# Performance work log

Measured on AMD Instinct MI355X. Metric: run time of the kernel, lower is better.

Reference implementation:

```python
import jax, jax.numpy as jnp
import numpy as np

EMB = 1024
E = 8        # num_experts
TOPK = 2
HID = 2048   # expert_dim

def setup_inputs() -> dict:
    key = jax.random.key(0)
    ks = jax.random.split(key, 10)
    s = lambda fan_in: 1.0 / np.sqrt(fan_in)
    x  = jax.random.normal(ks[0], (2, 2048, EMB), dtype=jnp.float32)
    Wr = jax.random.normal(ks[1], (EMB, E), dtype=jnp.float32) * s(EMB)
    br = jnp.zeros((E,), dtype=jnp.float32)
    # stacked expert weights, stored (in, out) so y = x @ W + b
    W1 = jax.random.normal(ks[2], (E, EMB, HID), dtype=jnp.float32) * s(EMB)
    b1 = jax.random.normal(ks[3], (E, HID), dtype=jnp.float32) * 0.01
    Wg = jax.random.normal(ks[4], (E, HID, HID), dtype=jnp.float32) * s(HID)
    bg = jax.random.normal(ks[5], (E, HID), dtype=jnp.float32) * 0.01
    W2 = jax.random.normal(ks[6], (E, HID, EMB), dtype=jnp.float32) * s(HID)
    b2 = jax.random.normal(ks[7], (E, EMB), dtype=jnp.float32) * 0.01
    return {"x": x, "Wr": Wr, "br": br, "W1": W1, "b1": b1,
            "Wg": Wg, "bg": bg, "W2": W2, "b2": b2}

def reference(x, Wr, br, W1, b1, Wg, bg, W2, b2):
    B, S, D = x.shape
    xt = x.reshape(B * S, D)                                  # [T, D]
    logits = xt @ Wr + br                                     # [T, E]
    probs = jax.nn.softmax(logits, axis=-1)
    topk_p, topk_i = jax.lax.top_k(probs, TOPK)               # [T, K]
    # dense gate matrix (top-k probs, NOT renormalized, as in source)
    gates = jnp.sum(jax.nn.one_hot(topk_i, E, dtype=xt.dtype) * topk_p[..., None], axis=1)  # [T, E]
    # expert MLP: layer1 (no act) -> relu(linear) -> layer2, for all experts
    h = jnp.einsum('td,edh->teh', xt, W1) + b1                # [T, E, HID]
    h = jax.nn.relu(jnp.einsum('teh,ehg->teg', h, Wg) + bg)   # [T, E, HID]
    y = jnp.einsum('teh,ehd->ted', h, W2) + b2                # [T, E, D]
    out = jnp.einsum('te,ted->td', gates, y)                  # weighted combine
    return out.reshape(B, S, D)
```

## Files before the change

### kernel.cpp

```cpp
#include <hip/hip_runtime.h>
#include <hip/hip_bf16.h>
#include <stdint.h>

#define NTOK 4096
#define EMBD 1024
#define NEXP 8
#define HIDD 2048
#define NPAIR (NTOK * 2)

typedef __attribute__((ext_vector_type(8))) __bf16 bf16x8;
typedef __attribute__((ext_vector_type(4))) float f32x4;

union V16 { uint4 u; bf16x8 b; };

__device__ __forceinline__ uint16_t f2bf(float f) {
    uint32_t u = __float_as_uint(f);
    return (uint16_t)((u + 0x7FFFu + ((u >> 16) & 1u)) >> 16);
}
__device__ __forceinline__ float bf2f(uint16_t u) {
    return __uint_as_float(((uint32_t)u) << 16);
}
__device__ __forceinline__ void gl_lds16(const uint16_t* g, uint16_t* l) {
    __builtin_amdgcn_global_load_lds(
        (const __attribute__((address_space(1))) void*)g,
        (__attribute__((address_space(3))) void*)l, 16, 0, 0);
}

#define W1_TILES 4096
#define WG_TILES 8192
#define W2_TILES 4096
__global__ __launch_bounds__(256) void transcast3_kernel(
    const float* __restrict__ W1, const float* __restrict__ Wg,
    const float* __restrict__ W2, uint16_t* __restrict__ W1t,
    uint16_t* __restrict__ Wgt, uint16_t* __restrict__ W2t) {
    int id = blockIdx.x;
    const float* src; uint16_t* dst; int K, N;
    if (id < W1_TILES) { src = W1; dst = W1t; K = EMBD; N = HIDD; }
    else if (id < W1_TILES + WG_TILES) { id -= W1_TILES; src = Wg; dst = Wgt; K = HIDD; N = HIDD; }
    else { id -= W1_TILES + WG_TILES; src = W2; dst = W2t; K = HIDD; N = EMBD; }
    int tn = N >> 6, tk = K >> 6;
    int per_e = tn * tk;
    int e = id / per_e, r = id % per_e;
    int n0 = (r % tn) * 64, k0 = (r / tn) * 64;

    __shared__ uint16_t tile[64][68];
    const float* S = src + ((size_t)e * K + k0) * N + n0;
    uint16_t* D = dst + ((size_t)e * N + n0) * K + k0;
    int t = threadIdx.x;
    int rn = (t & 15) * 4, rk = t >> 4;
#pragma unroll
    for (int p = 0; p < 4; p++) {
        int k = rk + p * 16;
        float4 v = *(const float4*)(S + (size_t)k * N + rn);
        ushort4 o;
        o.x = f2bf(v.x); o.y = f2bf(v.y); o.z = f2bf(v.z); o.w = f2bf(v.w);
        *(ushort4*)&tile[k][rn] = o;
    }
    __syncthreads();
    int wn = t >> 3, wk = (t & 7) * 8;
#pragma unroll
    for (int p = 0; p < 2; p++) {
        int n = wn + p * 32;
        uint32_t w0 = (uint32_t)tile[wk + 0][n] | ((uint32_t)tile[wk + 1][n] << 16);
        uint32_t w1 = (uint32_t)tile[wk + 2][n] | ((uint32_t)tile[wk + 3][n] << 16);
        uint32_t w2 = (uint32_t)tile[wk + 4][n] | ((uint32_t)tile[wk + 5][n] << 16);
        uint32_t w3 = (uint32_t)tile[wk + 6][n] | ((uint32_t)tile[wk + 7][n] << 16);
        uint4 pk = {w0, w1, w2, w3};
        *(uint4*)(D + (size_t)n * K + wk) = pk;
    }
}

__global__ __launch_bounds__(64) void router_kernel(const float* __restrict__ x,
                                                    const float* __restrict__ Wr,
                                                    const float* __restrict__ br,
                                                    uint16_t* __restrict__ xb,
                                                    int* __restrict__ counts,
                                                    int* __restrict__ pair_e,
                                                    float* __restrict__ pair_p) {
    int tok = blockIdx.x;
    int lane = threadIdx.x;
    const float* xr = x + (size_t)tok * EMBD;
    uint16_t* xbr = xb + (size_t)tok * EMBD;
    float acc[NEXP];
#pragma unroll
    for (int e = 0; e < NEXP; e++) acc[e] = 0.f;
    for (int d = lane; d < EMBD; d += 64) {
        float xv = xr[d];
        xbr[d] = f2bf(xv);
#pragma unroll
        for (int e = 0; e < NEXP; e++) acc[e] += xv * Wr[d * NEXP + e];
    }
#pragma unroll
    for (int e = 0; e < NEXP; e++) {
#pragma unroll
        for (int off = 32; off > 0; off >>= 1)
            acc[e] += __shfl_down(acc[e], off, 64);
    }
    if (lane == 0) {
        float lg[NEXP];
#pragma unroll
        for (int e = 0; e < NEXP; e++) lg[e] = acc[e] + br[e];
        int e0 = 0;
#pragma unroll
        for (int e = 1; e < NEXP; e++) if (lg[e] > lg[e0]) e0 = e;
        int e1 = (e0 == 0) ? 1 : 0;
#pragma unroll
        for (int e = 0; e < NEXP; e++) if (e != e0 && lg[e] > lg[e1]) e1 = e;
        float mx = lg[0];
#pragma unroll
        for (int e = 1; e < NEXP; e++) mx = fmaxf(mx, lg[e]);
        float s = 0.f, p[NEXP];
#pragma unroll
        for (int e = 0; e < NEXP; e++) { p[e] = __expf(lg[e] - mx); s += p[e]; }
        float inv = 1.f / s;
        pair_e[tok * 2 + 0] = e0; pair_p[tok * 2 + 0] = p[e0] * inv;
        pair_e[tok * 2 + 1] = e1; pair_p[tok * 2 + 1] = p[e1] * inv;
        atomicAdd(&counts[e0], 1);
        atomicAdd(&counts[e1], 1);
    }
}

__global__ __launch_bounds__(256) void scatter_kernel(const int* __restrict__ pair_e,
                                                      const int* __restrict__ counts,
                                                      int* __restrict__ cursors,
                                                      int* __restrict__ toklist,
                                                      int* __restrict__ posmap) {
    int i = blockIdx.x * 256 + threadIdx.x;
    int e = pair_e[i];
    int offs = 0;
    for (int j = 0; j < NEXP; j++) offs += (j < e) ? counts[j] : 0;
    int pos = offs + atomicAdd(&cursors[e], 1);
    toklist[pos] = i >> 1;
    posmap[i] = pos;
}

template <int KDIM, int NDIM, bool GATHER_A, bool RELU>
__global__ __launch_bounds__(256) void gemm_kernel(
    const uint16_t* __restrict__ Abase, const uint16_t* __restrict__ Btbase,
    const float* __restrict__ bbase, uint16_t* __restrict__ Out,
    const int* __restrict__ counts, const int* __restrict__ toklist) {
    int e = blockIdx.z;
    int offs = 0;
    for (int j = 0; j < NEXP; j++) offs += (j < e) ? counts[j] : 0;
    int n_e = counts[e];
    int m0 = blockIdx.y * 128;
    if (m0 >= n_e) return;
    int n0 = blockIdx.x * 128;
    const uint16_t* Bt = Btbase + (size_t)e * NDIM * KDIM;

    __shared__ uint16_t As[128 * 32];
    __shared__ uint16_t Bs[128 * 32];

    int tid = threadIdx.x;
    int lane = tid & 63;
    int wave = tid >> 6;

    int sr = tid >> 2;
    int ss = tid & 3;
    const uint16_t* arp[2];
    const uint16_t* brp[2];
#pragma unroll
    for (int p = 0; p < 2; p++) {
        int r = p * 64 + sr;
        int gs = ss ^ ((r >> 1) & 3);
        int grow;
        if (GATHER_A) {
            int idx = m0 + r;
            if (idx >= n_e) idx = 0;
            grow = toklist[offs + idx];
        } else {
            grow = offs + m0 + r;
        }
        arp[p] = Abase + (size_t)grow * KDIM + gs * 8;
        brp[p] = Bt + (size_t)(n0 + r) * KDIM + gs * 8;
    }
    uint16_t* alds[2] = { &As[wave * 512], &As[2048 + wave * 512] };
    uint16_t* blds[2] = { &Bs[wave * 512], &Bs[2048 + wave * 512] };

    int wm = (wave >> 1) * 64;
    int wn = (wave & 1) * 64;
    int l16 = lane & 15, qd = lane >> 4;
    const uint16_t* afp[4];
    const uint16_t* bfp[4];
#pragma unroll
    for (int t = 0; t < 4; t++) {
        int ar = wm + t * 16 + l16;
        afp[t] = &As[ar * 32 + (qd ^ ((ar >> 1) & 3)) * 8];
        int br = wn + t * 16 + l16;
        bfp[t] = &Bs[br * 32 + (qd ^ ((br >> 1) & 3)) * 8];
    }

    f32x4 acc[4][4];
    f32x4 zero = {0.f, 0.f, 0.f, 0.f};
#pragma unroll
    for (int i = 0; i < 4; i++)
#pragma unroll
        for (int j = 0; j < 4; j++) acc[i][j] = zero;

    for (int kb = 0; kb < KDIM; kb += 32) {
#pragma unroll
        for (int p = 0; p < 2; p++) {
            gl_lds16(arp[p] + kb, alds[p]);
            gl_lds16(brp[p] + kb, blds[p]);
        }
        __syncthreads();
        V16 af[4], bf[4];
#pragma unroll
        for (int t = 0; t < 4; t++) {
            af[t].u = *(const uint4*)(afp[t]);
            bf[t].u = *(const uint4*)(bfp[t]);
        }
#pragma unroll
        for (int i = 0; i < 4; i++)
#pragma unroll
            for (int j = 0; j < 4; j++)
                acc[i][j] = __builtin_amdgcn_mfma_f32_16x16x32_bf16(
                    af[i].b, bf[j].b, acc[i][j], 0, 0, 0);
        __syncthreads();
    }

    const float* bias = bbase + (size_t)e * NDIM;
    int mrem = n_e - m0;
#pragma unroll
    for (int i = 0; i < 4; i++) {
        int rb = wm + i * 16 + qd * 4;
#pragma unroll
        for (int j = 0; j < 4; j++) {
            int col = n0 + wn + j * 16 + l16;
            float bv = bias[col];
#pragma unroll
            for (int r = 0; r < 4; r++) {
                int lr = rb + r;
                if (lr < mrem) {
                    float v = acc[i][j][r] + bv;
                    if (RELU) v = fmaxf(v, 0.f);
                    Out[(size_t)(offs + m0 + lr) * NDIM + col] = f2bf(v);
                }
            }
        }
    }
}

__global__ __launch_bounds__(256) void combine_kernel(const uint16_t* __restrict__ y,
                                                      const int* __restrict__ posmap,
                                                      const float* __restrict__ pair_p,
                                                      float* __restrict__ out) {
    int t = blockIdx.x;
    int d4 = threadIdx.x;
    int p0 = posmap[t * 2], p1 = posmap[t * 2 + 1];
    float w0 = pair_p[t * 2], w1 = pair_p[t * 2 + 1];
    ushort4 a = ((const ushort4*)(y + (size_t)p0 * EMBD))[d4];
    ushort4 b = ((const ushort4*)(y + (size_t)p1 * EMBD))[d4];
    float4 o;
    o.x = w0 * bf2f(a.x) + w1 * bf2f(b.x);
    o.y = w0 * bf2f(a.y) + w1 * bf2f(b.y);
    o.z = w0 * bf2f(a.z) + w1 * bf2f(b.z);
    o.w = w0 * bf2f(a.w) + w1 * bf2f(b.w);
    ((float4*)(out + (size_t)t * EMBD))[d4] = o;
}

extern "C" void kernel_launch(void* const* d_in, const int* in_sizes, int n_in,
                              void* d_out, int out_size, void* d_ws, size_t ws_size,
                              hipStream_t stream) {
    const float* x  = (const float*)d_in[0];
    const float* Wr = (const float*)d_in[1];
    const float* br = (const float*)d_in[2];
    const float* W1 = (const float*)d_in[3];
    const float* b1 = (const float*)d_in[4];
    const float* Wg = (const float*)d_in[5];
    const float* bg = (const float*)d_in[6];
    const float* W2 = (const float*)d_in[7];
    const float* b2 = (const float*)d_in[8];
    float* out = (float*)d_out;

    char* ws = (char*)d_ws;
    uint16_t* xb  = (uint16_t*)ws;
    uint16_t* h   = (uint16_t*)(ws + (8ull << 20));
    uint16_t* yb  = h;
    uint16_t* W1t = (uint16_t*)(ws + (40ull << 20));
    uint16_t* g   = W1t;
    uint16_t* Wgt = (uint16_t*)(ws + (72ull << 20));
    uint16_t* W2t = (uint16_t*)(ws + (136ull << 20));
    int* meta = (int*)(ws + (168ull << 20));
    int*   counts  = meta;
    int*   cursors = meta + 8;
    int*   pair_e  = meta + 16;
    int*   toklist = meta + 16 + NPAIR;
    int*   posmap  = meta + 16 + 2 * NPAIR;
    float* pair_p  = (float*)(meta + 16 + 3 * NPAIR);

    hipMemsetAsync(counts, 0, 16 * sizeof(int), stream);

    router_kernel<<<NTOK, 64, 0, stream>>>(x, Wr, br, xb, counts, pair_e, pair_p);
    transcast3_kernel<<<W1_TILES + WG_TILES + W2_TILES, 256, 0, stream>>>(
        W1, Wg, W2, W1t, Wgt, W2t);
    scatter_kernel<<<NPAIR / 256, 256, 0, stream>>>(pair_e, counts, cursors, toklist, posmap);

    gemm_kernel<EMBD, HIDD, true, false>
        <<<dim3(HIDD / 128, NTOK / 128, NEXP), 256, 0, stream>>>(
            xb, W1t, b1, h, counts, toklist);
    gemm_kernel<HIDD, HIDD, false, true>
        <<<dim3(HIDD / 128, NTOK / 128, NEXP), 256, 0, stream>>>(
            h, Wgt, bg, g, counts, toklist);
    gemm_kernel<HIDD, EMBD, false, false>
        <<<dim3(EMBD / 128, NTOK / 128, NEXP), 256, 0, stream>>>(
            g, W2t, b2, yb, counts, toklist);
    combine_kernel<<<NTOK, 256, 0, stream>>>(yb, posmap, pair_p, out);
}
```

Measured before the change: 737.1 us.

## Fuse fp32 weight cast and transpose into GEMM B-tile loading

Removes the separate pre-pass that cast and transposed every expert weight matrix to bf16 in workspace. Each GEMM block now reads the original fp32 weights, converts them to bf16 in registers and writes them transposed into a padded LDS tile, prefetching the next k-slice into registers. This avoids one full read and write pass over all weights, about 384 MB of traffic. In exchange each M-block re-reads fp32 weights, doubling per-block B bandwidth, and relies on L2/MALL reuse. The LDS writes are unswizzled, so bank conflicts are possible.

Result: slower. 804.9 us (+9.2%).

```diff
diff --git a/kernel.cpp b/kernel.cpp
--- a/kernel.cpp
+++ b/kernel.cpp
@@ -17,6 +17,9 @@
     uint32_t u = __float_as_uint(f);
     return (uint16_t)((u + 0x7FFFu + ((u >> 16) & 1u)) >> 16);
 }
+__device__ __forceinline__ uint32_t pk2bf(float a, float b) {
+    return (uint32_t)f2bf(a) | ((uint32_t)f2bf(b) << 16);
+}
 __device__ __forceinline__ float bf2f(uint16_t u) {
     return __uint_as_float(((uint32_t)u) << 16);
 }
@@ -24,50 +27,6 @@
     __builtin_amdgcn_global_load_lds(
         (const __attribute__((address_space(1))) void*)g,
         (__attribute__((address_space(3))) void*)l, 16, 0, 0);
-}
-
-#define W1_TILES 4096
-#define WG_TILES 8192
-#define W2_TILES 4096
-__global__ __launch_bounds__(256) void transcast3_kernel(
-    const float* __restrict__ W1, const float* __restrict__ Wg,
-    const float* __restrict__ W2, uint16_t* __restrict__ W1t,
-    uint16_t* __restrict__ Wgt, uint16_t* __restrict__ W2t) {
-    int id = blockIdx.x;
-    const float* src; uint16_t* dst; int K, N;
-    if (id < W1_TILES) { src = W1; dst = W1t; K = EMBD; N = HIDD; }
-    else if (id < W1_TILES + WG_TILES) { id -= W1_TILES; src = Wg; dst = Wgt; K = HIDD; N = HIDD; }
-    else { id -= W1_TILES + WG_TILES; src = W2; dst = W2t; K = HIDD; N = EMBD; }
-    int tn = N >> 6, tk = K >> 6;
-    int per_e = tn * tk;
-    int e = id / per_e, r = id % per_e;
-    int n0 = (r % tn) * 64, k0 = (r / tn) * 64;
-
-    __shared__ uint16_t tile[64][68];
-    const float* S = src + ((size_t)e * K + k0) * N + n0;
-    uint16_t* D = dst + ((size_t)e * N + n0) * K + k0;
-    int t = threadIdx.x;
-    int rn = (t & 15) * 4, rk = t >> 4;
-#pragma unroll
-    for (int p = 0; p < 4; p++) {
-        int k = rk + p * 16;
-        float4 v = *(const float4*)(S + (size_t)k * N + rn);
-        ushort4 o;
-        o.x = f2bf(v.x); o.y = f2bf(v.y); o.z = f2bf(v.z); o.w = f2bf(v.w);
-        *(ushort4*)&tile[k][rn] = o;
-    }
-    __syncthreads();
-    int wn = t >> 3, wk = (t & 7) * 8;
-#pragma unroll
-    for (int p = 0; p < 2; p++) {
-        int n = wn + p * 32;
-        uint32_t w0 = (uint32_t)tile[wk + 0][n] | ((uint32_t)tile[wk + 1][n] << 16);
-        uint32_t w1 = (uint32_t)tile[wk + 2][n] | ((uint32_t)tile[wk + 3][n] << 16);
-        uint32_t w2 = (uint32_t)tile[wk + 4][n] | ((uint32_t)tile[wk + 5][n] << 16);
-        uint32_t w3 = (uint32_t)tile[wk + 6][n] | ((uint32_t)tile[wk + 7][n] << 16);
-        uint4 pk = {w0, w1, w2, w3};
-        *(uint4*)(D + (size_t)n * K + wk) = pk;
-    }
 }
 
 __global__ __launch_bounds__(64) void router_kernel(const float* __restrict__ x,
@@ -136,7 +95,7 @@
 
 template <int KDIM, int NDIM, bool GATHER_A, bool RELU>
 __global__ __launch_bounds__(256) void gemm_kernel(
-    const uint16_t* __restrict__ Abase, const uint16_t* __restrict__ Btbase,
+    const uint16_t* __restrict__ Abase, const float* __restrict__ Wbase,
     const float* __restrict__ bbase, uint16_t* __restrict__ Out,
     const int* __restrict__ counts, const int* __restrict__ toklist) {
     int e = blockIdx.z;
@@ -146,10 +105,10 @@
     int m0 = blockIdx.y * 128;
     if (m0 >= n_e) return;
     int n0 = blockIdx.x * 128;
-    const uint16_t* Bt = Btbase + (size_t)e * NDIM * KDIM;
+    const float* W = Wbase + (size_t)e * KDIM * NDIM;
 
     __shared__ uint16_t As[128 * 32];
-    __shared__ uint16_t Bs[128 * 32];
+    __shared__ uint16_t Bs[128 * 36];
 
     int tid = threadIdx.x;
     int lane = tid & 63;
@@ -158,7 +117,6 @@
     int sr = tid >> 2;
     int ss = tid & 3;
     const uint16_t* arp[2];
-    const uint16_t* brp[2];
 #pragma unroll
     for (int p = 0; p < 2; p++) {
         int r = p * 64 + sr;
@@ -172,10 +130,13 @@
             grow = offs + m0 + r;
         }
         arp[p] = Abase + (size_t)grow * KDIM + gs * 8;
-        brp[p] = Bt + (size_t)(n0 + r) * KDIM + gs * 8;
     }
     uint16_t* alds[2] = { &As[wave * 512], &As[2048 + wave * 512] };
-    uint16_t* blds[2] = { &Bs[wave * 512], &Bs[2048 + wave * 512] };
+
+    int nq = tid & 31;
+    int kq = tid >> 5;
+    const float* Wp = W + (size_t)(kq * 4) * NDIM + n0 + nq * 4;
+    uint16_t* bwp = &Bs[(nq * 4) * 36 + kq * 4];
 
     int wm = (wave >> 1) * 64;
     int wn = (wave & 1) * 64;
@@ -187,7 +148,7 @@
         int ar = wm + t * 16 + l16;
         afp[t] = &As[ar * 32 + (qd ^ ((ar >> 1) & 3)) * 8];
         int br = wn + t * 16 + l16;
-        bfp[t] = &Bs[br * 32 + (qd ^ ((br >> 1) & 3)) * 8];
+        bfp[t] = &Bs[br * 36 + qd * 8];
     }
 
     f32x4 acc[4][4];
@@ -197,18 +158,39 @@
 #pragma unroll
         for (int j = 0; j < 4; j++) acc[i][j] = zero;
 
+    float4 breg[4];
+#pragma unroll
+    for (int j = 0; j < 4; j++)
+        breg[j] = *(const float4*)(Wp + (size_t)j * NDIM);
+
     for (int kb = 0; kb < KDIM; kb += 32) {
 #pragma unroll
-        for (int p = 0; p < 2; p++) {
-            gl_lds16(arp[p] + kb, alds[p]);
-            gl_lds16(brp[p] + kb, blds[p]);
-        }
+        for (int p = 0; p < 2; p++) gl_lds16(arp[p] + kb, alds[p]);
+#pragma unroll
+        for (int i = 0; i < 4; i++) {
+            uint2 d;
+            d.x = pk2bf(breg[0].x, breg[1].x);
+            d.y = pk2bf(breg[2].x, breg[3].x);
+            *(uint2*)(bwp + i * 36) = d;
+            float4 t0 = breg[0], t1 = breg[1], t2 = breg[2], t3 = breg[3];
+            breg[0] = make_float4(t0.y, t0.z, t0.w, t0.x);
+            breg[1] = make_float4(t1.y, t1.z, t1.w, t1.x);
+            breg[2] = make_float4(t2.y, t2.z, t2.w, t2.x);
+            breg[3] = make_float4(t3.y, t3.z, t3.w, t3.x);
+        }
+        int kbn = (kb + 32 < KDIM) ? kb + 32 : 0;
+        float4 bnext[4];
+#pragma unroll
+        for (int j = 0; j < 4; j++)
+            bnext[j] = *(const float4*)(Wp + (size_t)(kbn + j) * NDIM);
         __syncthreads();
         V16 af[4], bf[4];
 #pragma unroll
         for (int t = 0; t < 4; t++) {
             af[t].u = *(const uint4*)(afp[t]);
-            bf[t].u = *(const uint4*)(bfp[t]);
+            uint2 lo = *(const uint2*)(bfp[t]);
+            uint2 hi = *(const uint2*)(bfp[t] + 4);
+            bf[t].u = make_uint4(lo.x, lo.y, hi.x, hi.y);
         }
 #pragma unroll
         for (int i = 0; i < 4; i++)
@@ -217,6 +199,8 @@
                 acc[i][j] = __builtin_amdgcn_mfma_f32_16x16x32_bf16(
                     af[i].b, bf[j].b, acc[i][j], 0, 0, 0);
         __syncthreads();
+#pragma unroll
+        for (int j = 0; j < 4; j++) breg[j] = bnext[j];
     }
 
     const float* bias = bbase + (size_t)e * NDIM;
@@ -274,14 +258,11 @@
     float* out = (float*)d_out;
 
     char* ws = (char*)d_ws;
-    uint16_t* xb  = (uint16_t*)ws;
-    uint16_t* h   = (uint16_t*)(ws + (8ull << 20));
-    uint16_t* yb  = h;
-    uint16_t* W1t = (uint16_t*)(ws + (40ull << 20));
-    uint16_t* g   = W1t;
-    uint16_t* Wgt = (uint16_t*)(ws + (72ull << 20));
-    uint16_t* W2t = (uint16_t*)(ws + (136ull << 20));
-    int* meta = (int*)(ws + (168ull << 20));
+    uint16_t* xb = (uint16_t*)ws;
+    uint16_t* h  = (uint16_t*)(ws + (8ull << 20));
+    uint16_t* yb = h;
+    uint16_t* g  = (uint16_t*)(ws + (40ull << 20));
+    int* meta = (int*)(ws + (72ull << 20));
     int*   counts  = meta;
     int*   cursors = meta + 8;
     int*   pair_e  = meta + 16;
@@ -292,18 +273,16 @@
     hipMemsetAsync(counts, 0, 16 * sizeof(int), stream);
 
     router_kernel<<<NTOK, 64, 0, stream>>>(x, Wr, br, xb, counts, pair_e, pair_p);
-    transcast3_kernel<<<W1_TILES + WG_TILES + W2_TILES, 256, 0, stream>>>(
-        W1, Wg, W2, W1t, Wgt, W2t);
     scatter_kernel<<<NPAIR / 256, 256, 0, stream>>>(pair_e, counts, cursors, toklist, posmap);
 
     gemm_kernel<EMBD, HIDD, true, false>
         <<<dim3(HIDD / 128, NTOK / 128, NEXP), 256, 0, stream>>>(
-            xb, W1t, b1, h, counts, toklist);
+            xb, W1, b1, h, counts, toklist);
     gemm_kernel<HIDD, HIDD, false, true>
         <<<dim3(HIDD / 128, NTOK / 128, NEXP), 256, 0, stream>>>(
-            h, Wgt, bg, g, counts, toklist);
+            h, Wg, bg, g, counts, toklist);
     gemm_kernel<HIDD, EMBD, false, false>
         <<<dim3(EMBD / 128, NTOK / 128, NEXP), 256, 0, stream>>>(
-            g, W2t, b2, yb, counts, toklist);
+            g, W2, b2, yb, counts, toklist);
     combine_kernel<<<NTOK, 256, 0, stream>>>(yb, posmap, pair_p, out);
 }
```
